# Kernel optimization log

Hardware: AMD Instinct MI355X
Metric: run time of the kernel (lower is better)

## Reference

```python
import jax, jax.numpy as jnp
import numpy as np

B, T, H = 4, 4096, 1024


def setup_inputs() -> dict:
    key = jax.random.key(0)
    ks = jax.random.split(key, 10)
    W_STD = 0.02  # small init keeps the WKV denominator well-conditioned
    inp = {
        "x": jax.random.normal(ks[0], (B, T, H), dtype=jnp.float32),
        "time_decay": jnp.exp(-jax.random.uniform(ks[1], (H,), minval=0.5, maxval=1.5)),
        "time_mix_key": jax.random.uniform(ks[2], (H,)),
        "time_mix_value": jax.random.uniform(ks[3], (H,)),
        "time_mix_receptance": jax.random.uniform(ks[4], (H,)),
        "W_receptance": jax.random.normal(ks[5], (H, H)) * W_STD,
        "W_key": jax.random.normal(ks[6], (H, H)) * W_STD,
        "W_value": jax.random.normal(ks[7], (H, H)) * W_STD,
        "W_out": jax.random.normal(ks[8], (H, H)) * W_STD,
        "b_out": jax.random.normal(ks[9], (H,)) * W_STD,
    }
    return inp


def reference(x, time_decay, time_mix_key, time_mix_value, time_mix_receptance,
              W_receptance, W_key, W_value, W_out, b_out):
    # time_shift: shifted[:, t] = x[:, t-1], shifted[:, 0] = 0
    shifted = jnp.pad(x, ((0, 0), (1, 0), (0, 0)))[:, :-1]
    xs = x + shifted  # original applies SAME mix to x and shifted
    k = (xs * time_mix_key) @ W_key.T          # [B,T,H]
    v = (xs * time_mix_value) @ W_value.T      # [B,T,H]
    r = jax.nn.sigmoid((xs * time_mix_receptance) @ W_receptance.T)

    def step(carry, kv):
        num, den = carry                       # [B,H] each
        ck, cv = kv                            # [B,H]
        out = (num + time_decay * ck * den) / (den + time_decay * ck)
        ek = jnp.exp(ck)
        return (time_decay * num + ek * cv, time_decay * den + ek), out

    init = (jnp.ones_like(k[:, 0]), jnp.ones_like(k[:, 0]))
    kT = jnp.swapaxes(k, 0, 1)  # [T,B,H]
    vT = jnp.swapaxes(v, 0, 1)
    _, outT = jax.lax.scan(step, init, (kT, vT))
    out = jnp.swapaxes(outT, 0, 1)             # [B,T,H]
    return (r * out) @ W_out.T + b_out
```

## Files before the change

### kernel.cpp

```cpp
#include <hip/hip_runtime.h>

#define H_DIM 1024
#define T_DIM 4096
#define B_DIM 4
#define M_DIM (B_DIM * T_DIM)
#define SCAN_C 64
#define SCAN_W 48

typedef __attribute__((ext_vector_type(8))) short short8;
typedef __attribute__((ext_vector_type(4))) float f32x4;
typedef _Float16 half8 __attribute__((ext_vector_type(8)));

__device__ __forceinline__ unsigned short f2h(float f) {
  _Float16 h = (_Float16)f;
  return __builtin_bit_cast(unsigned short, h);
}
__device__ __forceinline__ float h2f(unsigned short u) {
  return (float)__builtin_bit_cast(_Float16, u);
}

__device__ __forceinline__ double fast_exp64(double x) {
  const double L2E = 1.4426950408889634074;
  const double LN2 = 0.69314718055994530942;
  double z = x * L2E;
  double n = rint(z);
  double y = (z - n) * LN2;
  double p = 2.7557319223985890653e-6;
  p = fma(p, y, 2.4801587301587301566e-5);
  p = fma(p, y, 1.9841269841269841253e-4);
  p = fma(p, y, 1.3888888888888889419e-3);
  p = fma(p, y, 8.3333333333333332177e-3);
  p = fma(p, y, 4.1666666666666664354e-2);
  p = fma(p, y, 1.6666666666666665741e-1);
  p = fma(p, y, 0.5);
  p = fma(p, y, 1.0);
  p = fma(p, y, 1.0);
  long long bits = ((long long)(1023 + (int)n)) << 52;
  return p * __longlong_as_double(bits);
}

__global__ void xs_split_kernel(const float* __restrict__ x,
                                unsigned short* __restrict__ xs1,
                                unsigned short* __restrict__ xs2,
                                int n4) {
  int i = blockIdx.x * blockDim.x + threadIdx.x;
  const int HV = H_DIM / 4;
  if (i >= n4) return;
  int m = i / HV;
  int t = m & (T_DIM - 1);
  float4 cur = reinterpret_cast<const float4*>(x)[i];
  float4 prev = make_float4(0.f, 0.f, 0.f, 0.f);
  if (t > 0) prev = reinterpret_cast<const float4*>(x)[i - HV];
  float s[4] = {cur.x + prev.x, cur.y + prev.y, cur.z + prev.z, cur.w + prev.w};
  unsigned short a1[4], a2[4];
#pragma unroll
  for (int q = 0; q < 4; ++q) {
    unsigned short h1 = f2h(s[q]);
    a1[q] = h1;
    a2[q] = f2h((s[q] - h2f(h1)) * 2048.0f);
  }
  reinterpret_cast<ushort4*>(xs1)[i] = make_ushort4(a1[0], a1[1], a1[2], a1[3]);
  reinterpret_cast<ushort4*>(xs2)[i] = make_ushort4(a2[0], a2[1], a2[2], a2[3]);
}

__global__ void wprep_kernel(const float* __restrict__ Wrec, const float* __restrict__ Wkey,
                             const float* __restrict__ Wval, const float* __restrict__ Wout,
                             const float* __restrict__ tmk, const float* __restrict__ tmv,
                             const float* __restrict__ tmr,
                             unsigned short* __restrict__ WK1H, unsigned short* __restrict__ WK2H,
                             unsigned short* __restrict__ WVRH,
                             unsigned short* __restrict__ WOH) {
  int i = blockIdx.x * blockDim.x + threadIdx.x;
  if (i >= H_DIM * H_DIM) return;
  int j = i & (H_DIM - 1);
  float wk = Wkey[i] * tmk[j];
  unsigned short k1 = f2h(wk);
  WK1H[i] = k1;
  WK2H[i] = f2h((wk - h2f(k1)) * 2048.0f);
  WVRH[i] = f2h(Wval[i] * tmv[j]);
  WVRH[H_DIM * H_DIM + i] = f2h(Wrec[i] * tmr[j]);
  WOH[i] = f2h(Wout[i]);
}

struct GemmPasses {
  const unsigned short* A[6];
  const unsigned short* B[6];
  float sc[6];
  int n;
};

#define GBAR() do { asm volatile("" ::: "memory"); __builtin_amdgcn_sched_barrier(0); \
                    __builtin_amdgcn_s_barrier(); \
                    __builtin_amdgcn_sched_barrier(0); asm volatile("" ::: "memory"); } while (0)
#define WAIT_VM6() asm volatile("s_waitcnt vmcnt(6)" ::: "memory")
#define WAIT_VM0() asm volatile("s_waitcnt vmcnt(0)" ::: "memory")

template <int DT>
__device__ __forceinline__ f32x4 mma(short8 a, short8 b, f32x4 c) {
  if constexpr (DT == 0)
    return __builtin_amdgcn_mfma_f32_16x16x32_bf16(a, b, c, 0, 0, 0);
  else
    return __builtin_amdgcn_mfma_f32_16x16x32_f16(
        __builtin_bit_cast(half8, a), __builtin_bit_cast(half8, b), c, 0, 0, 0);
}

__device__ __forceinline__ const unsigned short* selA(const GemmPasses& P, int p) {
  const unsigned short* r = P.A[0];
  if (p == 1) r = P.A[1];
  if (p == 2) r = P.A[2];
  if (p == 3) r = P.A[3];
  if (p == 4) r = P.A[4];
  if (p == 5) r = P.A[5];
  return r;
}
__device__ __forceinline__ const unsigned short* selB(const GemmPasses& P, int p) {
  const unsigned short* r = P.B[0];
  if (p == 1) r = P.B[1];
  if (p == 2) r = P.B[2];
  if (p == 3) r = P.B[3];
  if (p == 4) r = P.B[4];
  if (p == 5) r = P.B[5];
  return r;
}

__device__ __forceinline__ void stage_half(const unsigned short* base, int rowoff,
                                           int ktp, int kk, int slot,
                                           int wid, int lane, unsigned char* smem) {
#pragma unroll
  for (int i = 0; i < 2; ++i) {
    int row = wid * 32 + i * 16 + (lane >> 2);
    int kcol8 = (lane & 3) ^ ((row >> 1) & 3);
    const unsigned short* src = base + (size_t)(rowoff + row) * 1024
                                + ktp * 64 + kk * 32 + kcol8 * 8;
    unsigned int doff = (unsigned int)(slot * 16384 + wid * 2048 + i * 1024);
    __builtin_amdgcn_global_load_lds(
        (const __attribute__((address_space(1))) void*)src,
        (__attribute__((address_space(3))) void*)(smem + doff), 16, 0, 0);
  }
}

__device__ __forceinline__ short8 frag_ld(const unsigned char* smem, int slot, int row, int kg) {
  int byte = slot * 16384 + row * 64 + ((kg ^ ((row >> 1) & 3)) * 16);
  return *reinterpret_cast<const short8*>(smem + byte);
}

template <int DT>
__global__ __launch_bounds__(512, 2) void gemm256_kernel(GemmPasses P, void* __restrict__ Cout,
                                                         int N, int NT,
                                                         const float* __restrict__ bias,
                                                         int omode) {
  __shared__ __attribute__((aligned(16))) unsigned char smem[131072];
  const int tid = threadIdx.x;
  const int wid = tid >> 6;
  const int lane = tid & 63;
  const int wm = wid >> 2;
  const int wn = wid & 3;
  const int frow = lane & 15;
  const int kg = lane >> 4;
  const int nwg = gridDim.x * gridDim.y;
  const int wg = blockIdx.y * gridDim.x + blockIdx.x;
  const int swz = (wg & 7) * (nwg >> 3) + (wg >> 3);
  const int brow = (swz / gridDim.x) << 8;
  const int bcol = (swz % gridDim.x) << 8;

  f32x4 acc[8][4];
#pragma unroll
  for (int f = 0; f < 8; ++f)
#pragma unroll
    for (int c = 0; c < 4; ++c)
      acc[f][c] = (f32x4){0.f, 0.f, 0.f, 0.f};

  stage_half(selA(P, 0), brow, 0, 0, 0, wid, lane, smem);
  stage_half(selB(P, 0), bcol, 0, 0, 1, wid, lane, smem);
  stage_half(selA(P, 0), brow, 0, 1, 2, wid, lane, smem);
  stage_half(selB(P, 0), bcol, 0, 1, 3, wid, lane, smem);
  stage_half(selA(P, 0), brow, 1, 0, 4, wid, lane, smem);
  stage_half(selB(P, 0), bcol, 1, 0, 5, wid, lane, smem);
  stage_half(selA(P, 0), brow, 1, 1, 6, wid, lane, smem);
  WAIT_VM6();
  GBAR();

  for (int t = 0; t < NT; ++t) {
    if ((t & 15) == 0 && t != 0) {
      float s = P.sc[t >> 4];
      if (s != 1.0f) {
#pragma unroll
        for (int f = 0; f < 8; ++f)
#pragma unroll
          for (int c = 0; c < 4; ++c)
#pragma unroll
            for (int q = 0; q < 4; ++q)
              acc[f][c][q] *= s;
      }
    }
    const int cur4 = (t & 1) * 4;
    const int nxt4 = cur4 ^ 4;
    short8 a[4], b[4];
#pragma unroll
    for (int f = 0; f < 4; ++f) a[f] = frag_ld(smem, cur4 + 0, wm * 128 + f * 16 + frow, kg);
#pragma unroll
    for (int c = 0; c < 4; ++c) b[c] = frag_ld(smem, cur4 + 1, wn * 64 + c * 16 + frow, kg);
    if (t + 1 < NT) {
      int ts = t + 1;
      stage_half(selB(P, ts >> 4), bcol, ts & 15, 1, nxt4 + 3, wid, lane, smem);
    }
    GBAR();
    __builtin_amdgcn_s_setprio(1);
#pragma unroll
    for (int f = 0; f < 4; ++f)
#pragma unroll
      for (int c = 0; c < 4; ++c)
        acc[f][c] = mma<DT>(a[f], b[c], acc[f][c]);
    __builtin_amdgcn_s_setprio(0);
    GBAR();
#pragma unroll
    for (int f = 0; f < 4; ++f) a[f] = frag_ld(smem, cur4 + 0, wm * 128 + (f + 4) * 16 + frow, kg);
    if (t + 2 < NT) {
      int ts = t + 2;
      stage_half(selA(P, ts >> 4), brow, ts & 15, 0, cur4 + 0, wid, lane, smem);
    }
    GBAR();
    __builtin_amdgcn_s_setprio(1);
#pragma unroll
    for (int f = 0; f < 4; ++f)
#pragma unroll
      for (int c = 0; c < 4; ++c)
        acc[f + 4][c] = mma<DT>(a[f], b[c], acc[f + 4][c]);
    __builtin_amdgcn_s_setprio(0);
    GBAR();
#pragma unroll
    for (int f = 0; f < 4; ++f) a[f] = frag_ld(smem, cur4 + 2, wm * 128 + f * 16 + frow, kg);
#pragma unroll
    for (int c = 0; c < 4; ++c) b[c] = frag_ld(smem, cur4 + 3, wn * 64 + c * 16 + frow, kg);
    if (t + 2 < NT) {
      int ts = t + 2;
      stage_half(selB(P, ts >> 4), bcol, ts & 15, 0, cur4 + 1, wid, lane, smem);
    }
    GBAR();
    __builtin_amdgcn_s_setprio(1);
#pragma unroll
    for (int f = 0; f < 4; ++f)
#pragma unroll
      for (int c = 0; c < 4; ++c)
        acc[f][c] = mma<DT>(a[f], b[c], acc[f][c]);
    __builtin_amdgcn_s_setprio(0);
    GBAR();
#pragma unroll
    for (int f = 0; f < 4; ++f) a[f] = frag_ld(smem, cur4 + 2, wm * 128 + (f + 4) * 16 + frow, kg);
    if (t + 2 < NT) {
      int ts = t + 2;
      stage_half(selA(P, ts >> 4), brow, ts & 15, 1, cur4 + 2, wid, lane, smem);
    }
    WAIT_VM6();
    GBAR();
    __builtin_amdgcn_s_setprio(1);
#pragma unroll
    for (int f = 0; f < 4; ++f)
#pragma unroll
      for (int c = 0; c < 4; ++c)
        acc[f + 4][c] = mma<DT>(a[f], b[c], acc[f + 4][c]);
    __builtin_amdgcn_s_setprio(0);
    GBAR();
  }
  WAIT_VM0();

#pragma unroll
  for (int f = 0; f < 8; ++f) {
    int r0 = brow + wm * 128 + f * 16 + kg * 4;
#pragma unroll
    for (int c = 0; c < 4; ++c) {
      int cc = bcol + wn * 64 + c * 16 + frow;
      if (omode == 0) {
        float bb = bias ? bias[cc] : 0.f;
        float* C = (float*)Cout;
#pragma unroll
        for (int q = 0; q < 4; ++q)
          C[(size_t)(r0 + q) * N + cc] = acc[f][c][q] + bb;
      } else {
        unsigned short* C = (unsigned short*)Cout;
#pragma unroll
        for (int q = 0; q < 4; ++q)
          C[(size_t)(r0 + q) * N + cc] = f2h(acc[f][c][q]);
      }
    }
  }
}

__global__ void wkv_scan_kernel(const float* __restrict__ kbuf,
                                const unsigned short* __restrict__ vrbuf,
                                const float* __restrict__ tdec,
                                unsigned short* __restrict__ rwh) {
  const int h = blockIdx.x * 64 + threadIdx.x;
  const int chunk = blockIdx.y;
  const int b = blockIdx.z;
  const int t0 = chunk * SCAN_C;
  const int tstart = (chunk == 0) ? 0 : (t0 - SCAN_W);
  const int tend = t0 + SCAN_C;
  double num, den;
  if (chunk == 0) { num = 1.0; den = 1.0; } else { num = 0.0; den = 0.0; }
  const double w = (double)tdec[h];
  size_t ik = ((size_t)b * T_DIM + tstart) * H_DIM + h;
  size_t iv = ((size_t)b * T_DIM + tstart) * 2048 + h;
  float kc = kbuf[ik];
  unsigned short vc = vrbuf[iv];
  unsigned short rc = vrbuf[iv + 1024];
  for (int t = tstart; t < tend; ++t) {
    int adv = (t + 1 < tend) ? 1 : 0;
    float kn = kbuf[ik + adv * H_DIM];
    unsigned short vn = vrbuf[iv + adv * 2048];
    unsigned short rn = vrbuf[iv + adv * 2048 + 1024];
    double ck = (double)kc;
    if (t >= t0) {
      double p = w * ck;
      double A = fma(p, den, num);
      double Bd = den + p;
      float outf = (float)A / (float)Bd;
      float rr = 1.0f / (1.0f + __expf(-h2f(rc)));
      rwh[ik] = f2h(rr * outf);
    }
    double ek = fast_exp64(ck);
    num = fma(w, num, ek * (double)h2f(vc));
    den = fma(w, den, ek);
    kc = kn; vc = vn; rc = rn;
    ik += H_DIM; iv += 2048;
  }
}

template <int DT>
static inline void run_gemm(const GemmPasses& P, void* C, int Mrows, int N,
                            const float* bias, int omode, hipStream_t stream) {
  gemm256_kernel<DT><<<dim3(N / 256, Mrows / 256), dim3(512), 0, stream>>>(
      P, C, N, P.n * 16, bias, omode);
}

extern "C" void kernel_launch(void* const* d_in, const int* in_sizes, int n_in,
                              void* d_out, int out_size, void* d_ws, size_t ws_size,
                              hipStream_t stream) {
  const float* x    = (const float*)d_in[0];
  const float* tdec = (const float*)d_in[1];
  const float* tmk  = (const float*)d_in[2];
  const float* tmv  = (const float*)d_in[3];
  const float* tmr  = (const float*)d_in[4];
  const float* Wrec = (const float*)d_in[5];
  const float* Wkey = (const float*)d_in[6];
  const float* Wval = (const float*)d_in[7];
  const float* Wout = (const float*)d_in[8];
  const float* bout = (const float*)d_in[9];
  float* out = (float*)d_out;
  unsigned char* ws = (unsigned char*)d_ws;

  const size_t W2 = (size_t)H_DIM * H_DIM * 2;
  const size_t BF_FULL = (size_t)M_DIM * H_DIM * 2;
  const size_t NEED = 2 * BF_FULL + 2 * BF_FULL + 5 * W2;
  if (ws_size < NEED) return;

  size_t off = 0;
  unsigned short* XS1H = (unsigned short*)(ws + off); off += BF_FULL;
  unsigned short* XS2H = (unsigned short*)(ws + off); off += BF_FULL;
  unsigned short* VR   = (unsigned short*)(ws + off); off += 2 * BF_FULL;
  unsigned short* WK1H = (unsigned short*)(ws + off); off += W2;
  unsigned short* WK2H = (unsigned short*)(ws + off); off += W2;
  unsigned short* WVRH = (unsigned short*)(ws + off); off += 2 * W2;
  unsigned short* WOH  = (unsigned short*)(ws + off); off += W2;

  wprep_kernel<<<dim3(H_DIM * H_DIM / 256), dim3(256), 0, stream>>>(
      Wrec, Wkey, Wval, Wout, tmk, tmv, tmr, WK1H, WK2H, WVRH, WOH);

  int n4 = M_DIM * (H_DIM / 4);
  xs_split_kernel<<<dim3(n4 / 256), dim3(256), 0, stream>>>(x, XS1H, XS2H, n4);

  GemmPasses Pvr;
  Pvr.n = 1;
  Pvr.A[0] = XS1H; Pvr.B[0] = WVRH; Pvr.sc[0] = 1.f;
  for (int p = 1; p < 6; ++p) { Pvr.A[p] = XS1H; Pvr.B[p] = WVRH; Pvr.sc[p] = 1.f; }
  run_gemm<1>(Pvr, VR, M_DIM, 2 * H_DIM, nullptr, 2, stream);

  const float S11 = 0.00048828125f;
  GemmPasses Pk;
  Pk.n = 4;
  Pk.A[0] = XS2H; Pk.B[0] = WK2H; Pk.sc[0] = 1.f;
  Pk.A[1] = XS1H; Pk.B[1] = WK2H; Pk.sc[1] = S11;
  Pk.A[2] = XS2H; Pk.B[2] = WK1H; Pk.sc[2] = 1.f;
  Pk.A[3] = XS1H; Pk.B[3] = WK1H; Pk.sc[3] = S11;
  Pk.A[4] = XS1H; Pk.B[4] = WK1H; Pk.sc[4] = 1.f;
  Pk.A[5] = XS1H; Pk.B[5] = WK1H; Pk.sc[5] = 1.f;
  run_gemm<1>(Pk, out, M_DIM, H_DIM, nullptr, 0, stream);

  unsigned short* RWH = XS1H;
  wkv_scan_kernel<<<dim3(H_DIM / 64, T_DIM / SCAN_C, B_DIM), dim3(64), 0, stream>>>(
      out, VR, tdec, RWH);

  GemmPasses Po;
  Po.n = 1;
  Po.A[0] = RWH; Po.B[0] = WOH; Po.sc[0] = 1.f;
  for (int p = 1; p < 6; ++p) { Po.A[p] = RWH; Po.B[p] = WOH; Po.sc[p] = 1.f; }
  run_gemm<1>(Po, out, M_DIM, H_DIM, bout, 0, stream);
}
```

Baseline: 362.1 us.

## Fuse split-precision key GEMM passes into one kernel sharing A/B tiles

Replaces the four-pass split-fp16 key projection, which re-streamed the A and B operands once per pass through the generic 256x256 GEMM, with a dedicated 256x128-tile kernel. It stages the hi/lo parts of X and W together into a triple-buffered LDS pipeline and computes all four cross products per K-step with two accumulator sets, combining them with a final scale at writeback. This cuts global and LDS traffic for the key GEMM roughly in half. It costs more LDS (144KB), more accumulator registers, and pre-scales the lo-lo term in fp16, which could affect precision slightly.

```diff
diff --git a/kernel.cpp b/kernel.cpp
--- a/kernel.cpp
+++ b/kernel.cpp
@@ -82,46 +82,167 @@
   WOH[i] = f2h(Wout[i]);
 }
 
-struct GemmPasses {
-  const unsigned short* A[6];
-  const unsigned short* B[6];
-  float sc[6];
-  int n;
-};
-
 #define GBAR() do { asm volatile("" ::: "memory"); __builtin_amdgcn_sched_barrier(0); \
                     __builtin_amdgcn_s_barrier(); \
                     __builtin_amdgcn_sched_barrier(0); asm volatile("" ::: "memory"); } while (0)
 #define WAIT_VM6() asm volatile("s_waitcnt vmcnt(6)" ::: "memory")
 #define WAIT_VM0() asm volatile("s_waitcnt vmcnt(0)" ::: "memory")
 
-template <int DT>
-__device__ __forceinline__ f32x4 mma(short8 a, short8 b, f32x4 c) {
-  if constexpr (DT == 0)
-    return __builtin_amdgcn_mfma_f32_16x16x32_bf16(a, b, c, 0, 0, 0);
-  else
-    return __builtin_amdgcn_mfma_f32_16x16x32_f16(
-        __builtin_bit_cast(half8, a), __builtin_bit_cast(half8, b), c, 0, 0, 0);
-}
-
-__device__ __forceinline__ const unsigned short* selA(const GemmPasses& P, int p) {
-  const unsigned short* r = P.A[0];
-  if (p == 1) r = P.A[1];
-  if (p == 2) r = P.A[2];
-  if (p == 3) r = P.A[3];
-  if (p == 4) r = P.A[4];
-  if (p == 5) r = P.A[5];
-  return r;
-}
-__device__ __forceinline__ const unsigned short* selB(const GemmPasses& P, int p) {
-  const unsigned short* r = P.B[0];
-  if (p == 1) r = P.B[1];
-  if (p == 2) r = P.B[2];
-  if (p == 3) r = P.B[3];
-  if (p == 4) r = P.B[4];
-  if (p == 5) r = P.B[5];
-  return r;
-}
+__device__ __forceinline__ f32x4 mma_h(short8 a, short8 b, f32x4 c) {
+  return __builtin_amdgcn_mfma_f32_16x16x32_f16(
+      __builtin_bit_cast(half8, a), __builtin_bit_cast(half8, b), c, 0, 0, 0);
+}
+__device__ __forceinline__ f32x4 mma_hh(half8 a, short8 b, f32x4 c) {
+  return __builtin_amdgcn_mfma_f32_16x16x32_f16(a, __builtin_bit_cast(half8, b), c, 0, 0, 0);
+}
+
+__device__ __forceinline__ void stage_A32(const unsigned short* base, int rowoff, int kt,
+                                          unsigned sbase, int wid, int lane,
+                                          unsigned char* smem) {
+#pragma unroll
+  for (int i = 0; i < 2; ++i) {
+    int row = wid * 32 + i * 16 + (lane >> 2);
+    int col8 = (lane & 3) ^ ((row >> 1) & 3);
+    const unsigned short* src = base + (size_t)(rowoff + row) * 1024 + kt * 32 + col8 * 8;
+    __builtin_amdgcn_global_load_lds(
+        (const __attribute__((address_space(1))) void*)src,
+        (__attribute__((address_space(3))) void*)(smem + sbase + wid * 2048 + i * 1024), 16, 0, 0);
+  }
+}
+__device__ __forceinline__ void stage_B32(const unsigned short* base, int coloff, int kt,
+                                          unsigned sbase, int wid, int lane,
+                                          unsigned char* smem) {
+  int row = wid * 16 + (lane >> 2);
+  int col8 = (lane & 3) ^ ((row >> 1) & 3);
+  const unsigned short* src = base + (size_t)(coloff + row) * 1024 + kt * 32 + col8 * 8;
+  __builtin_amdgcn_global_load_lds(
+      (const __attribute__((address_space(1))) void*)src,
+      (__attribute__((address_space(3))) void*)(smem + sbase + wid * 1024), 16, 0, 0);
+}
+__device__ __forceinline__ short8 frag_ld2(const unsigned char* smem, unsigned rbase,
+                                           int row, int kg) {
+  return *reinterpret_cast<const short8*>(smem + rbase + row * 64 + ((kg ^ ((row >> 1) & 3)) * 16));
+}
+
+__global__ __launch_bounds__(512, 2) void gemm_k_kernel(
+    const unsigned short* __restrict__ A1, const unsigned short* __restrict__ A2,
+    const unsigned short* __restrict__ B1, const unsigned short* __restrict__ B2,
+    float* __restrict__ C) {
+  __shared__ __attribute__((aligned(16))) unsigned char smem[147456];
+  const int tid = threadIdx.x;
+  const int wid = tid >> 6;
+  const int lane = tid & 63;
+  const int wm = wid >> 2;
+  const int wn = wid & 3;
+  const int frow = lane & 15;
+  const int kg = lane >> 4;
+  const int nwg = gridDim.x * gridDim.y;
+  const int wg = blockIdx.y * gridDim.x + blockIdx.x;
+  const int swz = (wg & 7) * (nwg >> 3) + (wg >> 3);
+  const int brow = (swz / gridDim.x) << 8;
+  const int bcol = (swz % gridDim.x) << 7;
+
+  f32x4 acc0[8][2], acc1[8][2];
+#pragma unroll
+  for (int f = 0; f < 8; ++f)
+#pragma unroll
+    for (int c = 0; c < 2; ++c) {
+      acc0[f][c] = (f32x4){0.f, 0.f, 0.f, 0.f};
+      acc1[f][c] = (f32x4){0.f, 0.f, 0.f, 0.f};
+    }
+
+  const int NT = 32;
+#pragma unroll
+  for (int t0 = 0; t0 < 2; ++t0) {
+    unsigned sb = t0 * 49152u;
+    stage_A32(A1, brow, t0, sb + 0u, wid, lane, smem);
+    stage_A32(A2, brow, t0, sb + 16384u, wid, lane, smem);
+    stage_B32(B1, bcol, t0, sb + 32768u, wid, lane, smem);
+    stage_B32(B2, bcol, t0, sb + 40960u, wid, lane, smem);
+  }
+  WAIT_VM6();
+  GBAR();
+
+  for (int t = 0; t < NT; ++t) {
+    unsigned sb = (unsigned)(t % 3) * 49152u;
+    unsigned st = (unsigned)((t + 2) % 3) * 49152u;
+    const bool stg = (t + 2 < NT);
+    short8 a1[8], a2[8], b1[2], b2[2];
+#pragma unroll
+    for (int f = 0; f < 8; ++f) a1[f] = frag_ld2(smem, sb, wm * 128 + f * 16 + frow, kg);
+#pragma unroll
+    for (int c = 0; c < 2; ++c) b1[c] = frag_ld2(smem, sb + 32768u, wn * 32 + c * 16 + frow, kg);
+    if (stg) stage_A32(A1, brow, t + 2, st + 0u, wid, lane, smem);
+    GBAR();
+    __builtin_amdgcn_s_setprio(1);
+#pragma unroll
+    for (int f = 0; f < 8; ++f)
+#pragma unroll
+      for (int c = 0; c < 2; ++c)
+        acc0[f][c] = mma_h(a1[f], b1[c], acc0[f][c]);
+    __builtin_amdgcn_s_setprio(0);
+    GBAR();
+#pragma unroll
+    for (int c = 0; c < 2; ++c) b2[c] = frag_ld2(smem, sb + 40960u, wn * 32 + c * 16 + frow, kg);
+    if (stg) stage_A32(A2, brow, t + 2, st + 16384u, wid, lane, smem);
+    GBAR();
+    __builtin_amdgcn_s_setprio(1);
+#pragma unroll
+    for (int f = 0; f < 8; ++f)
+#pragma unroll
+      for (int c = 0; c < 2; ++c)
+        acc1[f][c] = mma_h(a1[f], b2[c], acc1[f][c]);
+    __builtin_amdgcn_s_setprio(0);
+    GBAR();
+#pragma unroll
+    for (int f = 0; f < 8; ++f) a2[f] = frag_ld2(smem, sb + 16384u, wm * 128 + f * 16 + frow, kg);
+    if (stg) {
+      stage_B32(B1, bcol, t + 2, st + 32768u, wid, lane, smem);
+      stage_B32(B2, bcol, t + 2, st + 40960u, wid, lane, smem);
+    }
+    GBAR();
+    __builtin_amdgcn_s_setprio(1);
+#pragma unroll
+    for (int f = 0; f < 8; ++f)
+#pragma unroll
+      for (int c = 0; c < 2; ++c)
+        acc1[f][c] = mma_h(a2[f], b1[c], acc1[f][c]);
+    __builtin_amdgcn_s_setprio(0);
+    GBAR();
+    WAIT_VM6();
+    GBAR();
+    __builtin_amdgcn_s_setprio(1);
+#pragma unroll
+    for (int f = 0; f < 8; ++f) {
+      half8 ad = __builtin_bit_cast(half8, a2[f]) * (_Float16)0.00048828125f;
+#pragma unroll
+      for (int c = 0; c < 2; ++c)
+        acc1[f][c] = mma_hh(ad, b2[c], acc1[f][c]);
+    }
+    __builtin_amdgcn_s_setprio(0);
+    GBAR();
+  }
+  WAIT_VM0();
+
+#pragma unroll
+  for (int f = 0; f < 8; ++f) {
+    int r0 = brow + wm * 128 + f * 16 + kg * 4;
+#pragma unroll
+    for (int c = 0; c < 2; ++c) {
+      int cc = bcol + wn * 32 + c * 16 + frow;
+#pragma unroll
+      for (int q = 0; q < 4; ++q)
+        C[(size_t)(r0 + q) * H_DIM + cc] =
+            fmaf(0.00048828125f, acc1[f][c][q], acc0[f][c][q]);
+    }
+  }
+}
+
+struct GemmPasses {
+  const unsigned short* A[2];
+  const unsigned short* B[2];
+  int n;
+};
 
 __device__ __forceinline__ void stage_half(const unsigned short* base, int rowoff,
                                            int ktp, int kk, int slot,
@@ -138,13 +259,11 @@
         (__attribute__((address_space(3))) void*)(smem + doff), 16, 0, 0);
   }
 }
-
 __device__ __forceinline__ short8 frag_ld(const unsigned char* smem, int slot, int row, int kg) {
   int byte = slot * 16384 + row * 64 + ((kg ^ ((row >> 1) & 3)) * 16);
   return *reinterpret_cast<const short8*>(smem + byte);
 }
 
-template <int DT>
 __global__ __launch_bounds__(512, 2) void gemm256_kernel(GemmPasses P, void* __restrict__ Cout,
                                                          int N, int NT,
                                                          const float* __restrict__ bias,
@@ -170,31 +289,23 @@
     for (int c = 0; c < 4; ++c)
       acc[f][c] = (f32x4){0.f, 0.f, 0.f, 0.f};
 
-  stage_half(selA(P, 0), brow, 0, 0, 0, wid, lane, smem);
-  stage_half(selB(P, 0), bcol, 0, 0, 1, wid, lane, smem);
-  stage_half(selA(P, 0), brow, 0, 1, 2, wid, lane, smem);
-  stage_half(selB(P, 0), bcol, 0, 1, 3, wid, lane, smem);
-  stage_half(selA(P, 0), brow, 1, 0, 4, wid, lane, smem);
-  stage_half(selB(P, 0), bcol, 1, 0, 5, wid, lane, smem);
-  stage_half(selA(P, 0), brow, 1, 1, 6, wid, lane, smem);
+  const unsigned short* Ag = P.A[0];
+  const unsigned short* Bg = P.B[0];
+  stage_half(Ag, brow, 0, 0, 0, wid, lane, smem);
+  stage_half(Bg, bcol, 0, 0, 1, wid, lane, smem);
+  stage_half(Ag, brow, 0, 1, 2, wid, lane, smem);
+  stage_half(Bg, bcol, 0, 1, 3, wid, lane, smem);
+  stage_half(Ag, brow, 1, 0, 4, wid, lane, smem);
+  stage_half(Bg, bcol, 1, 0, 5, wid, lane, smem);
+  stage_half(Ag, brow, 1, 1, 6, wid, lane, smem);
   WAIT_VM6();
   GBAR();
 
   for (int t = 0; t < NT; ++t) {
-    if ((t & 15) == 0 && t != 0) {
-      float s = P.sc[t >> 4];
-      if (s != 1.0f) {
-#pragma unroll
-        for (int f = 0; f < 8; ++f)
-#pragma unroll
-          for (int c = 0; c < 4; ++c)
-#pragma unroll
-            for (int q = 0; q < 4; ++q)
-              acc[f][c][q] *= s;
-      }
-    }
     const int cur4 = (t & 1) * 4;
     const int nxt4 = cur4 ^ 4;
+    const unsigned short* Agp = P.A[(t >> 4) >= P.n ? P.n - 1 : (t >> 4)];
+    const unsigned short* Bgp = P.B[(t >> 4) >= P.n ? P.n - 1 : (t >> 4)];
     short8 a[4], b[4];
 #pragma unroll
     for (int f = 0; f < 4; ++f) a[f] = frag_ld(smem, cur4 + 0, wm * 128 + f * 16 + frow, kg);
@@ -202,7 +313,7 @@
     for (int c = 0; c < 4; ++c) b[c] = frag_ld(smem, cur4 + 1, wn * 64 + c * 16 + frow, kg);
     if (t + 1 < NT) {
       int ts = t + 1;
-      stage_half(selB(P, ts >> 4), bcol, ts & 15, 1, nxt4 + 3, wid, lane, smem);
+      stage_half(P.B[(ts >> 4)], bcol, ts & 15, 1, nxt4 + 3, wid, lane, smem);
     }
     GBAR();
     __builtin_amdgcn_s_setprio(1);
@@ -210,14 +321,14 @@
     for (int f = 0; f < 4; ++f)
 #pragma unroll
       for (int c = 0; c < 4; ++c)
-        acc[f][c] = mma<DT>(a[f], b[c], acc[f][c]);
+        acc[f][c] = mma_h(a[f], b[c], acc[f][c]);
     __builtin_amdgcn_s_setprio(0);
     GBAR();
 #pragma unroll
     for (int f = 0; f < 4; ++f) a[f] = frag_ld(smem, cur4 + 0, wm * 128 + (f + 4) * 16 + frow, kg);
     if (t + 2 < NT) {
       int ts = t + 2;
-      stage_half(selA(P, ts >> 4), brow, ts & 15, 0, cur4 + 0, wid, lane, smem);
+      stage_half(P.A[(ts >> 4)], brow, ts & 15, 0, cur4 + 0, wid, lane, smem);
     }
     GBAR();
     __builtin_amdgcn_s_setprio(1);
@@ -225,7 +336,7 @@
     for (int f = 0; f < 4; ++f)
 #pragma unroll
       for (int c = 0; c < 4; ++c)
-        acc[f + 4][c] = mma<DT>(a[f], b[c], acc[f + 4][c]);
+        acc[f + 4][c] = mma_h(a[f], b[c], acc[f + 4][c]);
     __builtin_amdgcn_s_setprio(0);
     GBAR();
 #pragma unroll
@@ -234,7 +345,7 @@
     for (int c = 0; c < 4; ++c) b[c] = frag_ld(smem, cur4 + 3, wn * 64 + c * 16 + frow, kg);
     if (t + 2 < NT) {
       int ts = t + 2;
-      stage_half(selB(P, ts >> 4), bcol, ts & 15, 0, cur4 + 1, wid, lane, smem);
+      stage_half(P.B[(ts >> 4)], bcol, ts & 15, 0, cur4 + 1, wid, lane, smem);
     }
     GBAR();
     __builtin_amdgcn_s_setprio(1);
@@ -242,14 +353,14 @@
     for (int f = 0; f < 4; ++f)
 #pragma unroll
       for (int c = 0; c < 4; ++c)
-        acc[f][c] = mma<DT>(a[f], b[c], acc[f][c]);
+        acc[f][c] = mma_h(a[f], b[c], acc[f][c]);
     __builtin_amdgcn_s_setprio(0);
     GBAR();
 #pragma unroll
     for (int f = 0; f < 4; ++f) a[f] = frag_ld(smem, cur4 + 2, wm * 128 + (f + 4) * 16 + frow, kg);
     if (t + 2 < NT) {
       int ts = t + 2;
-      stage_half(selA(P, ts >> 4), brow, ts & 15, 1, cur4 + 2, wid, lane, smem);
+      stage_half(P.A[(ts >> 4)], brow, ts & 15, 1, cur4 + 2, wid, lane, smem);
     }
     WAIT_VM6();
     GBAR();
@@ -258,7 +369,7 @@
     for (int f = 0; f < 4; ++f)
 #pragma unroll
       for (int c = 0; c < 4; ++c)
-        acc[f + 4][c] = mma<DT>(a[f], b[c], acc[f + 4][c]);
+        acc[f + 4][c] = mma_h(a[f], b[c], acc[f + 4][c]);
     __builtin_amdgcn_s_setprio(0);
     GBAR();
   }
@@ -326,10 +437,9 @@
   }
 }
 
-template <int DT>
-static inline void run_gemm(const GemmPasses& P, void* C, int Mrows, int N,
-                            const float* bias, int omode, hipStream_t stream) {
-  gemm256_kernel<DT><<<dim3(N / 256, Mrows / 256), dim3(512), 0, stream>>>(
+static inline void run_gemm256(const GemmPasses& P, void* C, int Mrows, int N,
+                               const float* bias, int omode, hipStream_t stream) {
+  gemm256_kernel<<<dim3(N / 256, Mrows / 256), dim3(512), 0, stream>>>(
       P, C, N, P.n * 16, bias, omode);
 }
 
@@ -371,20 +481,11 @@
 
   GemmPasses Pvr;
   Pvr.n = 1;
-  Pvr.A[0] = XS1H; Pvr.B[0] = WVRH; Pvr.sc[0] = 1.f;
-  for (int p = 1; p < 6; ++p) { Pvr.A[p] = XS1H; Pvr.B[p] = WVRH; Pvr.sc[p] = 1.f; }
-  run_gemm<1>(Pvr, VR, M_DIM, 2 * H_DIM, nullptr, 2, stream);
-
-  const float S11 = 0.00048828125f;
-  GemmPasses Pk;
-  Pk.n = 4;
-  Pk.A[0] = XS2H; Pk.B[0] = WK2H; Pk.sc[0] = 1.f;
-  Pk.A[1] = XS1H; Pk.B[1] = WK2H; Pk.sc[1] = S11;
-  Pk.A[2] = XS2H; Pk.B[2] = WK1H; Pk.sc[2] = 1.f;
-  Pk.A[3] = XS1H; Pk.B[3] = WK1H; Pk.sc[3] = S11;
-  Pk.A[4] = XS1H; Pk.B[4] = WK1H; Pk.sc[4] = 1.f;
-  Pk.A[5] = XS1H; Pk.B[5] = WK1H; Pk.sc[5] = 1.f;
-  run_gemm<1>(Pk, out, M_DIM, H_DIM, nullptr, 0, stream);
+  Pvr.A[0] = XS1H; Pvr.B[0] = WVRH; Pvr.A[1] = XS1H; Pvr.B[1] = WVRH;
+  run_gemm256(Pvr, VR, M_DIM, 2 * H_DIM, nullptr, 2, stream);
+
+  gemm_k_kernel<<<dim3(H_DIM / 128, M_DIM / 256), dim3(512), 0, stream>>>(
+      XS1H, XS2H, WK1H, WK2H, out);
 
   unsigned short* RWH = XS1H;
   wkv_scan_kernel<<<dim3(H_DIM / 64, T_DIM / SCAN_C, B_DIM), dim3(64), 0, stream>>>(
@@ -392,7 +493,6 @@
 
   GemmPasses Po;
   Po.n = 1;
-  Po.A[0] = RWH; Po.B[0] = WOH; Po.sc[0] = 1.f;
-  for (int p = 1; p < 6; ++p) { Po.A[p] = RWH; Po.B[p] = WOH; Po.sc[p] = 1.f; }
-  run_gemm<1>(Po, out, M_DIM, H_DIM, bout, 0, stream);
-}
+  Po.A[0] = RWH; Po.B[0] = WOH; Po.A[1] = RWH; Po.B[1] = WOH;
+  run_gemm256(Po, out, M_DIM, H_DIM, bout, 0, stream);
+}
```

After: 338.2 us. 1.07x faster.
